# Optimization experiments

Measured on AMD Instinct MI355X. Metric: run time of the kernel, lower is better.

## Reference

```python
import jax, jax.numpy as jnp
import numpy as np

B, NA, NE = 1024, 15, 16
N_AGENTS = NA + 1
BN = B * N_AGENTS
D_OWN = D_ALL = D_EN = 32
H, NH, NMOVE, RD = 256, 4, 6, 8
HD = H // NH
GATE = 1.0
NEG = -1e9  # stand-in for -inf (safe under autodiff)


def _gelu(x):
    return jax.nn.gelu(x, approximate=False)  # torch nn.GELU default is exact


def _ln(x, g, b, eps=1e-5):
    m = x.mean(-1, keepdims=True)
    v = ((x - m) ** 2).mean(-1, keepdims=True)
    return (x - m) * jax.lax.rsqrt(v + eps) * g + b


def _masked_mean(x, mask, axis):
    w = mask[..., None].astype(x.dtype)
    return (x * w).sum(axis) / jnp.clip(w.sum(axis), 1e-8)


def _mha(q, kv, mask, Wq, Wk, Wv, Wo):
    # q: [BN,H], kv: [BN,M,H], mask: [BN,M] bool
    bn = q.shape[0]
    qh = (q @ Wq.T).reshape(bn, NH, HD)
    kh = (kv @ Wk.T).reshape(bn, -1, NH, HD)
    vh = (kv @ Wv.T).reshape(bn, -1, NH, HD)
    scores = jnp.einsum('bhd,bmhd->bhm', qh, kh) / np.sqrt(HD)
    scores = jnp.where(mask[:, None, :], scores, NEG)
    attn = jax.nn.softmax(scores, axis=-1)
    ctx = jnp.einsum('bhm,bmhd->bhd', attn, vh).reshape(bn, H)
    return ctx @ Wo.T


def setup_inputs() -> dict:
    key = jax.random.key(0)
    ks = iter(jax.random.split(key, 64))
    nrm = lambda *s: jax.random.normal(next(ks), s, dtype=jnp.float32)
    w = lambda o, i: nrm(o, i) * 0.02
    inp = dict(
        bs=B,
        own_feats=nrm(BN, 1, D_OWN),
        ally_feats=nrm(BN, NA, D_ALL),
        enemy_feats=nrm(BN, NE, D_EN),
        hidden_state=nrm(B, N_AGENTS, H),
        own_W=w(H, D_OWN), own_b=jnp.zeros(H),
        ally_W=w(H, D_ALL), ally_b=jnp.zeros(H),
        en_W=w(H, D_EN), en_b=jnp.zeros(H),
        aA_Wq=w(H, H), aA_Wk=w(H, H), aA_Wv=w(H, H), aA_Wo=w(H, H),
        aE_Wq=w(H, H), aE_Wk=w(H, H), aE_Wv=w(H, H), aE_Wo=w(H, H),
        fuse_W1=w(H, 3 * H), fuse_b1=jnp.zeros(H), fuse_g1=jnp.ones(H), fuse_be1=jnp.zeros(H),
        fuse_W2=w(H, H), fuse_b2=jnp.zeros(H),
        pool_W1=w(128, 3 * H), pool_b1=jnp.zeros(128), pool_g1=jnp.ones(128), pool_be1=jnp.zeros(128),
        pool_W2=w(128, 128), pool_b2=jnp.zeros(128),
        role_W1=w(128, 128), role_b1=jnp.zeros(128), role_g1=jnp.ones(128), role_be1=jnp.zeros(128),
        role_W2=w(RD, 128), role_b2=jnp.zeros(RD),
        rln_g=jnp.ones(RD), rln_b=jnp.zeros(RD),
        gru_Wih=w(3 * H, H + RD), gru_Whh=w(3 * H, H),
        gru_bih=jnp.zeros(3 * H), gru_bhh=jnp.zeros(3 * H),
        qn_W=w(NMOVE, H), qn_b=jnp.zeros(NMOVE),
        qp_W=w(H, H + RD), kp_W=w(H, H),
    )
    return inp


def reference(bs, own_feats, ally_feats, enemy_feats, hidden_state,
              own_W, own_b, ally_W, ally_b, en_W, en_b,
              aA_Wq, aA_Wk, aA_Wv, aA_Wo, aE_Wq, aE_Wk, aE_Wv, aE_Wo,
              fuse_W1, fuse_b1, fuse_g1, fuse_be1, fuse_W2, fuse_b2,
              pool_W1, pool_b1, pool_g1, pool_be1, pool_W2, pool_b2,
              role_W1, role_b1, role_g1, role_be1, role_W2, role_b2,
              rln_g, rln_b, gru_Wih, gru_Whh, gru_bih, gru_bhh,
              qn_W, qn_b, qp_W, kp_W):
    ally_mask = ~jnp.all(ally_feats == 0, axis=-1)   # [BN,Na]
    enemy_mask = ~jnp.all(enemy_feats == 0, axis=-1)  # [BN,Ne]

    own_e = own_feats @ own_W.T + own_b        # [BN,1,H]
    ally_e = ally_feats @ ally_W.T + ally_b    # [BN,Na,H]
    enemy_e = enemy_feats @ en_W.T + en_b      # [BN,Ne,H]
    self_emb = own_e[:, 0]                     # [BN,H]

    cA = _mha(self_emb, ally_e, ally_mask, aA_Wq, aA_Wk, aA_Wv, aA_Wo)
    cE = _mha(self_emb, enemy_e, enemy_mask, aE_Wq, aE_Wk, aE_Wv, aE_Wo)

    # fuse MLP: Linear -> GELU -> LN -> Linear
    f_in = jnp.concatenate([self_emb, cA, cE], axis=-1)
    h0 = _ln(_gelu(f_in @ fuse_W1.T + fuse_b1), fuse_g1, fuse_be1) @ fuse_W2.T + fuse_b2

    pA = _masked_mean(ally_e, ally_mask, 1)
    pE = _masked_mean(enemy_e, enemy_mask, 1)
    p_in = jnp.concatenate([self_emb, pA, pE], axis=-1)
    pooled = _ln(_gelu(p_in @ pool_W1.T + pool_b1), pool_g1, pool_be1) @ pool_W2.T + pool_b2
    r = jnp.tanh(_ln(_gelu(pooled @ role_W1.T + role_b1), role_g1, role_be1) @ role_W2.T + role_b2)
    r = _ln(r, rln_g, rln_b)

    # GRUCell (torch convention)
    h_prev = hidden_state.reshape(-1, H)
    x = jnp.concatenate([h0, GATE * r], axis=-1)
    gi = x @ gru_Wih.T + gru_bih
    gh = h_prev @ gru_Whh.T + gru_bhh
    i_r, i_z, i_n = jnp.split(gi, 3, axis=-1)
    h_r, h_z, h_n = jnp.split(gh, 3, axis=-1)
    rg = jax.nn.sigmoid(i_r + h_r)
    zg = jax.nn.sigmoid(i_z + h_z)
    ng = jnp.tanh(i_n + rg * h_n)
    h_cur = (1.0 - zg) * ng + zg * h_prev

    q_normal = h_cur @ qn_W.T + qn_b  # [BN,n_move]

    q_vec = jnp.concatenate([h_cur, GATE * r], axis=-1) @ qp_W.T  # [BN,H]
    k_vec = enemy_e @ kp_W.T                                       # [BN,Ne,H]
    logits = jnp.einsum('bj,bmj->bm', q_vec, k_vec) / np.sqrt(H)
    logits = jnp.where(enemy_mask, logits, NEG)
    denom = jnp.clip(enemy_mask.sum(-1, keepdims=True), 1).astype(logits.dtype)
    mean_valid = jnp.where(enemy_mask, logits, 0.0).sum(-1, keepdims=True) / denom
    q_interact = logits - mean_valid

    Q = jnp.concatenate([q_normal, q_interact], axis=-1)
    h_out = h_cur.reshape(bs, N_AGENTS, H)
    return Q, h_out
```

## Files before the change

kernel.cpp:

```cpp
#include <hip/hip_runtime.h>
#include <hip/hip_bf16.h>


#define MROWS 16384

typedef __attribute__((ext_vector_type(8))) short short8;
typedef __attribute__((ext_vector_type(4))) float float4v;
typedef __attribute__((ext_vector_type(4))) unsigned short ushort4v;
typedef __attribute__((ext_vector_type(2))) unsigned short ushort2v;

__device__ __forceinline__ unsigned short f2b(float f) {
    __hip_bfloat16 h = __float2bfloat16(f);
    return *reinterpret_cast<unsigned short*>(&h);
}
__device__ __forceinline__ float b2f(unsigned short u) {
    __hip_bfloat16 h;
    *reinterpret_cast<unsigned short*>(&h) = u;
    return __bfloat162float(h);
}
__device__ __forceinline__ void gll16(const unsigned short* g, unsigned short* l) {
    __builtin_amdgcn_global_load_lds((const __attribute__((address_space(1))) void*)g,
                                     (__attribute__((address_space(3))) void*)l, 16, 0, 0);
}

__global__ void cvt_misc(const float* __restrict__ hidden, const float* __restrict__ ownf,
                         unsigned short* __restrict__ XG, unsigned short* __restrict__ OWNb,
                         unsigned short* __restrict__ zbuf) {
    int idx = blockIdx.x * 256 + threadIdx.x;
    const int nh = MROWS * 64;
    const int no = MROWS * 8;
    if (idx < nh) {
        int row = idx >> 6, c4 = (idx & 63) * 4;
        float4 v = *(const float4*)(hidden + (size_t)row * 256 + c4);
        ushort4v d = { f2b(v.x), f2b(v.y), f2b(v.z), f2b(v.w) };
        *(ushort4v*)(XG + (size_t)row * 520 + 264 + c4) = d;
    } else if (idx < nh + no) {
        int j = idx - nh;
        int row = j >> 3, c4 = (j & 7) * 4;
        float4 v = *(const float4*)(ownf + (size_t)row * 32 + c4);
        ushort4v d = { f2b(v.x), f2b(v.y), f2b(v.z), f2b(v.w) };
        *(ushort4v*)(OWNb + (size_t)row * 32 + c4) = d;
    } else if (idx < nh + no + 16) {
        int j = idx - nh - no;
        ((uint4*)zbuf)[j] = make_uint4(0u, 0u, 0u, 0u);
    }
}

struct TOp {
    int type;
    const float* A; int sAi, sAk;
    const float* B; int sBj, sBk;
    void* O; int sOi;
    int I, J, K;
    int nb; int aB, bB, oB;
};
struct TOpSet { int n; int tiles[26]; TOp ops[26]; };

__global__ __launch_bounds__(256)
void compose_tiled(TOpSet S) {
    int t = blockIdx.x;
    int op = 0;
    while (op < S.n && t >= S.tiles[op]) { t -= S.tiles[op]; op++; }
    if (op >= S.n) return;
    TOp o = S.ops[op];
    int ti = (o.I + 31) >> 5, tj = (o.J + 31) >> 5;
    int per = ti * tj;
    int b = t / per;
    int rem = t - b * per;
    int i0 = (rem / tj) * 32, j0 = (rem % tj) * 32;
    int tid = threadIdx.x;
    if (o.type >= 2) {
        for (int e = tid; e < 1024; e += 256) {
            int r = e >> 5, c = e & 31;
            int i = i0 + r, j = j0 + c;
            if (i < o.I && j < o.J) {
                unsigned short v = 0;
                if (o.type == 2) v = f2b(o.A[(long)b * o.aB + (long)i * o.sAi + (long)j * o.sAk]);
                ((unsigned short*)o.O)[(long)b * o.oB + (long)i * o.sOi + j] = v;
            }
        }
        return;
    }
    __shared__ float As[32][33];
    __shared__ float Bs[32][33];
    int tx = tid & 15, ty = tid >> 4;
    float a00 = 0.f, a01 = 0.f, a10 = 0.f, a11 = 0.f;
    const float* Ab = o.A + (long)b * o.aB;
    const float* Bb = o.B + (long)b * o.bB;
    for (int k0 = 0; k0 < o.K; k0 += 32) {
        for (int e = tid; e < 1024; e += 256) {
            int r = e >> 5, c = e & 31;
            As[r][c] = (i0 + r < o.I && k0 + c < o.K)
                       ? Ab[(long)(i0 + r) * o.sAi + (long)(k0 + c) * o.sAk] : 0.f;
            Bs[r][c] = (k0 + r < o.K && j0 + c < o.J)
                       ? Bb[(long)(j0 + c) * o.sBj + (long)(k0 + r) * o.sBk] : 0.f;
        }
        __syncthreads();
#pragma unroll
        for (int k = 0; k < 32; k++) {
            float x0 = As[ty * 2][k], x1 = As[ty * 2 + 1][k];
            float y0 = Bs[k][tx * 2], y1 = Bs[k][tx * 2 + 1];
            a00 += x0 * y0; a01 += x0 * y1; a10 += x1 * y0; a11 += x1 * y1;
        }
        __syncthreads();
    }
    int i = i0 + ty * 2, j = j0 + tx * 2;
    float vals[2][2] = {{a00, a01}, {a10, a11}};
#pragma unroll
    for (int di = 0; di < 2; di++)
#pragma unroll
        for (int dj = 0; dj < 2; dj++) {
            int ii = i + di, jj = j + dj;
            if (ii < o.I && jj < o.J) {
                long oidx = (long)b * o.oB + (long)ii * o.sOi + jj;
                if (o.type == 0) ((unsigned short*)o.O)[oidx] = f2b(vals[di][dj]);
                else ((float*)o.O)[oidx] = vals[di][dj];
            }
        }
}

struct MOp { const float* A; int sAi; const float* x; const float* b1; const float* b2; float* out; int I, K; };
struct MOpSet { int n; int waves[10]; MOp ops[10]; };

__global__ void mv_ops(MOpSet S) {
    int wid = blockIdx.x * 4 + (threadIdx.x >> 6);
    int lane = threadIdx.x & 63;
    int op = 0;
    while (op < S.n && wid >= S.waves[op]) { wid -= S.waves[op]; op++; }
    if (op >= S.n) return;
    MOp o = S.ops[op];
    float s = 0.f;
    for (int k = lane; k < o.K; k += 64) s += o.A[(long)wid * o.sAi + k] * o.x[k];
    for (int off = 32; off; off >>= 1) s += __shfl_xor(s, off, 64);
    if (lane == 0) {
        if (o.b1) s += o.b1[wid];
        if (o.b2) s += o.b2[wid];
        o.out[wid] = s;
    }
}

template<int BM, int BN>
__global__ __launch_bounds__(256, 4)
void gemm_bf16(const unsigned short* __restrict__ A, int lda,
               const unsigned short* __restrict__ W,
               const float* __restrict__ bias,
               unsigned short* __restrict__ C, int ldc,
               int N, int K, int act,
               const unsigned short* __restrict__ zbuf) {
    constexpr int MI = BM / 32, NJ = BN / 32;
    __shared__ __align__(16) unsigned short As[2][BM * 32];
    __shared__ __align__(16) unsigned short Bs[2][BN * 32];
    int tid = threadIdx.x;
    int m0 = blockIdx.x * BM, n0 = blockIdx.y * BN;
    int wave = tid >> 6, lane = tid & 63;
    int wm = (wave & 1) * (BM / 2), wn = (wave >> 1) * (BN / 2);
    int l16 = lane & 15, quad = lane >> 4;

    float4v acc[MI][NJ];
#pragma unroll
    for (int i = 0; i < MI; i++)
#pragma unroll
        for (int j = 0; j < NJ; j++) acc[i][j] = (float4v){0.f, 0.f, 0.f, 0.f};

    int swz = ((l16 >> 1) & 3) * 8;
    int nt = (K + 31) >> 5;

    auto stage = [&](int buf, int k0) {
#pragma unroll
        for (int s0 = 0; s0 < BM * 4; s0 += 256) {
            int s = s0 + tid;
            int row = s >> 2;
            int cg = (s & 3) ^ ((row >> 1) & 3);
            int ka = k0 + cg * 8;
            gll16((ka < K) ? A + (size_t)(m0 + row) * lda + ka : zbuf, &As[buf][s * 8]);
        }
#pragma unroll
        for (int s0 = 0; s0 < BN * 4; s0 += 256) {
            int s = s0 + tid;
            int row = s >> 2;
            int cg = (s & 3) ^ ((row >> 1) & 3);
            int ka = k0 + cg * 8;
            gll16((ka < K && n0 + row < N) ? W + (size_t)(n0 + row) * K + ka : zbuf,
                  &Bs[buf][s * 8]);
        }
    };
    auto compute = [&](int buf) {
        short8 a[MI], b[NJ];
#pragma unroll
        for (int i = 0; i < MI; i++)
            a[i] = *(const short8*)(&As[buf][(wm + i * 16 + l16) * 32 + ((quad * 8) ^ swz)]);
#pragma unroll
        for (int j = 0; j < NJ; j++)
            b[j] = *(const short8*)(&Bs[buf][(wn + j * 16 + l16) * 32 + ((quad * 8) ^ swz)]);
#pragma unroll
        for (int i = 0; i < MI; i++)
#pragma unroll
            for (int j = 0; j < NJ; j++)
                acc[i][j] = __builtin_amdgcn_mfma_f32_16x16x32_bf16(a[i], b[j], acc[i][j], 0, 0, 0);
    };

    stage(0, 0);
    asm volatile("s_waitcnt vmcnt(0)" ::: "memory");
    __builtin_amdgcn_s_barrier();
    for (int t = 0; t < nt - 1; t++) {
        stage((t + 1) & 1, (t + 1) << 5);
        compute(t & 1);
        asm volatile("s_waitcnt vmcnt(0)" ::: "memory");
        __builtin_amdgcn_s_barrier();
    }
    compute((nt - 1) & 1);

#pragma unroll
    for (int i = 0; i < MI; i++) {
#pragma unroll
        for (int j = 0; j < NJ; j++) {
#pragma unroll
            for (int rr = 0; rr < 4; rr++) {
                int rowm = m0 + wm + i * 16 + quad * 4 + rr;
                int coln = wn + j * 16 + l16;
                if (n0 + coln >= N) continue;
                float v = acc[i][j][rr];
                if (bias) v += bias[n0 + coln];
                if (act == 1) v = 0.5f * v * (1.f + erff(v * 0.70710678f));
                C[(size_t)rowm * ldc + n0 + coln] = f2b(v);
            }
        }
    }
}

__global__ __launch_bounds__(256, 4)
void gemm_gru(const unsigned short* __restrict__ A, int lda,
              const unsigned short* __restrict__ W,
              const float* __restrict__ gbias,
              const float* __restrict__ hp,
              float* __restrict__ hout, unsigned short* __restrict__ XQ,
              int K, const unsigned short* __restrict__ zbuf) {
    __shared__ __align__(16) unsigned short As[2][64 * 32];
    __shared__ __align__(16) unsigned short Ws[2][4 * 64 * 32];
    int tid = threadIdx.x;
    int m0 = blockIdx.x * 64, n0 = blockIdx.y * 64;
    int wave = tid >> 6, lane = tid & 63;
    int wm = (wave & 1) * 32, wn = (wave >> 1) * 32;
    int l16 = lane & 15, quad = lane >> 4;

    float4v acc[4][2][2];
#pragma unroll
    for (int g = 0; g < 4; g++)
#pragma unroll
        for (int i = 0; i < 2; i++)
#pragma unroll
            for (int j = 0; j < 2; j++) acc[g][i][j] = (float4v){0.f, 0.f, 0.f, 0.f};

    int swz = ((l16 >> 1) & 3) * 8;
    int nt = (K + 31) >> 5;
    int srow = tid >> 2;
    int cg = (tid & 3) ^ ((srow >> 1) & 3);
    const unsigned short* Arow = A + (size_t)(m0 + srow) * lda + cg * 8;
    const unsigned short* Wrow[4];
#pragma unroll
    for (int g = 0; g < 4; g++)
        Wrow[g] = W + (size_t)(g * 256 + n0 + srow) * K + cg * 8;
    int kaOff = cg * 8;

    auto stage = [&](int buf, int k0) {
        int ka = k0 + kaOff;
        gll16((ka < K) ? Arow + k0 : zbuf, &As[buf][tid * 8]);
#pragma unroll
        for (int g = 0; g < 4; g++)
            gll16((ka < K) ? Wrow[g] + k0 : zbuf, &Ws[buf][(g * 256 + tid) * 8]);
    };
    auto compute = [&](int buf) {
        short8 a[2], b[4][2];
#pragma unroll
        for (int i = 0; i < 2; i++)
            a[i] = *(const short8*)(&As[buf][(wm + i * 16 + l16) * 32 + ((quad * 8) ^ swz)]);
#pragma unroll
        for (int g = 0; g < 4; g++)
#pragma unroll
            for (int j = 0; j < 2; j++)
                b[g][j] = *(const short8*)(&Ws[buf][g * 2048 + (wn + j * 16 + l16) * 32 + ((quad * 8) ^ swz)]);
#pragma unroll
        for (int g = 0; g < 4; g++)
#pragma unroll
            for (int i = 0; i < 2; i++)
#pragma unroll
                for (int j = 0; j < 2; j++)
                    acc[g][i][j] = __builtin_amdgcn_mfma_f32_16x16x32_bf16(a[i], b[g][j], acc[g][i][j], 0, 0, 0);
    };

    stage(0, 0);
    asm volatile("s_waitcnt vmcnt(0)" ::: "memory");
    __builtin_amdgcn_s_barrier();
    for (int t = 0; t < nt - 1; t++) {
        stage((t + 1) & 1, (t + 1) << 5);
        compute(t & 1);
        asm volatile("s_waitcnt vmcnt(0)" ::: "memory");
        __builtin_amdgcn_s_barrier();
    }
    compute((nt - 1) & 1);

#pragma unroll
    for (int i = 0; i < 2; i++) {
#pragma unroll
        for (int j = 0; j < 2; j++) {
#pragma unroll
            for (int rr = 0; rr < 4; rr++) {
                int rowm = m0 + wm + i * 16 + quad * 4 + rr;
                int coln = n0 + wn + j * 16 + l16;
                float r_ = acc[0][i][j][rr] + gbias[coln];
                float z_ = acc[1][i][j][rr] + gbias[256 + coln];
                float in_ = acc[2][i][j][rr] + gbias[512 + coln];
                float hn_ = acc[3][i][j][rr] + gbias[768 + coln];
                float rg = 1.f / (1.f + __expf(-r_));
                float zg = 1.f / (1.f + __expf(-z_));
                float ng = tanhf(in_ + rg * hn_);
                float h = (1.f - zg) * ng + zg * hp[(size_t)rowm * 256 + coln];
                hout[(size_t)rowm * 256 + coln] = h;
                XQ[(size_t)rowm * 264 + coln] = f2b(h);
            }
        }
    }
}

__global__ __launch_bounds__(256)
void ln_fp(const unsigned short* __restrict__ FPC,
           const float* __restrict__ g1, const float* __restrict__ be1,
           const float* __restrict__ g2, const float* __restrict__ be2,
           unsigned short* __restrict__ XG, unsigned short* __restrict__ T2) {
    int tid = threadIdx.x;
    size_t row = (size_t)blockIdx.x * 4 + (tid >> 6);
    int l = tid & 63;
    const unsigned short* src = FPC + row * 384;
    ushort4v vf = *(const ushort4v*)(src + l * 4);
    ushort2v vp = *(const ushort2v*)(src + 256 + l * 2);
    float f0 = b2f(vf[0]), f1 = b2f(vf[1]), f2v = b2f(vf[2]), f3 = b2f(vf[3]);
    float p0 = b2f(vp[0]), p1 = b2f(vp[1]);
    float s = f0 + f1 + f2v + f3;
    float q = f0 * f0 + f1 * f1 + f2v * f2v + f3 * f3;
    float s2 = p0 + p1, q2 = p0 * p0 + p1 * p1;
    for (int o = 32; o; o >>= 1) {
        s += __shfl_xor(s, o, 64); q += __shfl_xor(q, o, 64);
        s2 += __shfl_xor(s2, o, 64); q2 += __shfl_xor(q2, o, 64);
    }
    float mean = s * (1.f / 256.f);
    float rstd = rsqrtf(q * (1.f / 256.f) - mean * mean + 1e-5f);
    float4 g = *(const float4*)(g1 + l * 4);
    float4 be = *(const float4*)(be1 + l * 4);
    ushort4v o4;
    o4[0] = f2b((f0 - mean) * rstd * g.x + be.x);
    o4[1] = f2b((f1 - mean) * rstd * g.y + be.y);
    o4[2] = f2b((f2v - mean) * rstd * g.z + be.z);
    o4[3] = f2b((f3 - mean) * rstd * g.w + be.w);
    *(ushort4v*)(XG + row * 520 + l * 4) = o4;
    float mean2 = s2 * (1.f / 128.f);
    float rstd2 = rsqrtf(q2 * (1.f / 128.f) - mean2 * mean2 + 1e-5f);
    float2 gg = *(const float2*)(g2 + l * 2);
    float2 bb = *(const float2*)(be2 + l * 2);
    ushort2v o2;
    o2[0] = f2b((p0 - mean2) * rstd2 * gg.x + bb.x);
    o2[1] = f2b((p1 - mean2) * rstd2 * gg.y + bb.y);
    *(ushort2v*)(T2 + row * 128 + l * 2) = o2;
}

__global__ __launch_bounds__(256)
void glue_attn(const float* __restrict__ allyf, const float* __restrict__ enemyf,
               const float* __restrict__ ownf, const unsigned short* __restrict__ QKS,
               unsigned short* __restrict__ X) {
    __shared__ __align__(16) float af[4][540];
    __shared__ __align__(16) float ef[4][576];
    __shared__ __align__(16) float qk[4][288];
    __shared__ float attnA[4][64];
    __shared__ float attnE[4][64];
    __shared__ float mskA[4][16];
    __shared__ float mskE[4][16];
    int tid = threadIdx.x;
    size_t rb = (size_t)blockIdx.x * 4;

    for (int idx = tid; idx < 480; idx += 256) {
        int r = idx / 120, ch = idx - r * 120;
        float4 v = *(const float4*)(allyf + ((rb + r) * 480 + ch * 4));
        *(float4*)&af[r][(ch >> 3) * 36 + (ch & 7) * 4] = v;
    }
    for (int idx = tid; idx < 512; idx += 256) {
        int r = idx >> 7, ch = idx & 127;
        float4 v = *(const float4*)(enemyf + ((rb + r) * 512 + ch * 4));
        *(float4*)&ef[r][(ch >> 3) * 36 + (ch & 7) * 4] = v;
    }
    if (tid < 128) {
        int r = tid >> 5, ch = tid & 31;
        short8 v = *(const short8*)(QKS + (rb + r) * 256 + ch * 8);
#pragma unroll
        for (int j = 0; j < 8; j++)
            qk[r][(ch >> 2) * 36 + (ch & 3) * 8 + j] = b2f((unsigned short)v[j]);
    } else {
        int r = (tid - 128) >> 5, c = (tid - 128) & 31;
        X[(rb + r) * 360 + c] = f2b(ownf[(rb + r) * 32 + c]);
    }
    if (tid < 24) {
        int r = tid / 6, c = 98 + tid % 6;
        X[(rb + r) * 360 + c] = 0;
    }
    __syncthreads();

    if (tid < 248) {
        int pair = tid >> 1, half = tid & 1;
        int r = pair / 31, e = pair - r * 31;
        const float* base = (e < 15) ? &af[r][e * 36] : &ef[r][(e - 15) * 36];
        const float4* b4 = (const float4*)base + half * 4;
        bool nz = false;
#pragma unroll
        for (int k = 0; k < 4; k++) {
            float4 v = b4[k];
            nz |= (v.x != 0.f) || (v.y != 0.f) || (v.z != 0.f) || (v.w != 0.f);
        }
        int other = __shfl_xor((int)nz, 1, 64);
        float mv = (nz || other != 0) ? 1.f : 0.f;
        if (half == 0) {
            if (e < 15) mskA[r][e] = mv; else mskE[r][e - 15] = mv;
        }
    } else if (tid < 252) {
        mskA[tid - 248][15] = 0.f;
    }
    __syncthreads();

    int r = tid >> 6, lane = tid & 63;
    int h = lane >> 4, m = lane & 15;
    {
        float sc = -3.0e38f;
        if (m < 15) {
            const float4* qa = (const float4*)&qk[r][h * 36];
            const float4* aa = (const float4*)&af[r][m * 36];
            float s = 0.f;
#pragma unroll
            for (int k = 0; k < 8; k++) {
                float4 q = qa[k], a = aa[k];
                s += q.x * a.x + q.y * a.y + q.z * a.z + q.w * a.w;
            }
            sc = (mskA[r][m] > 0.f) ? s * 0.125f : -1e9f;
        }
        float mx = sc;
        for (int o = 8; o; o >>= 1) mx = fmaxf(mx, __shfl_xor(mx, o, 64));
        float e = (m < 15) ? __expf(sc - mx) : 0.f;
        float sm = e;
        for (int o = 8; o; o >>= 1) sm += __shfl_xor(sm, o, 64);
        attnA[r][h * 16 + m] = e / sm;
    }
    {
        const float4* qa = (const float4*)&qk[r][(4 + h) * 36];
        const float4* aa = (const float4*)&ef[r][m * 36];
        float s = 0.f;
#pragma unroll
        for (int k = 0; k < 8; k++) {
            float4 q = qa[k], a = aa[k];
            s += q.x * a.x + q.y * a.y + q.z * a.z + q.w * a.w;
        }
        float sc = (mskE[r][m] > 0.f) ? s * 0.125f : -1e9f;
        float mx = sc;
        for (int o = 8; o; o >>= 1) mx = fmaxf(mx, __shfl_xor(mx, o, 64));
        float e = __expf(sc - mx);
        float sm = e;
        for (int o = 8; o; o >>= 1) sm += __shfl_xor(sm, o, 64);
        attnE[r][h * 16 + m] = e / sm;
    }
    __syncthreads();
    size_t row = rb + r;
#pragma unroll
    for (int it = 0; it < 2; it++) {
        int idx = lane + it * 64;
        int hh = idx >> 5, c = idx & 31;
        float sA = 0.f;
        for (int mm = 0; mm < 15; mm++) sA += attnA[r][hh * 16 + mm] * af[r][mm * 36 + c];
        X[row * 360 + 104 + idx] = f2b(sA);
        float sE = 0.f;
        for (int mm = 0; mm < 16; mm++) sE += attnE[r][hh * 16 + mm] * ef[r][mm * 36 + c];
        X[row * 360 + 232 + idx] = f2b(sE);
    }
    if (lane < 32) {
        float cnt = 0.f;
        for (int mm = 0; mm < 15; mm++) cnt += mskA[r][mm];
        float s = 0.f;
        for (int mm = 0; mm < 15; mm++) s += af[r][mm * 36 + lane];
        X[row * 360 + 32 + lane] = f2b(s / fmaxf(cnt, 1e-8f));
        if (lane == 0) X[row * 360 + 96] = f2b(cnt > 0.f ? 1.f : 0.f);
    } else {
        int c = lane - 32;
        float cnt = 0.f;
        for (int mm = 0; mm < 16; mm++) cnt += mskE[r][mm];
        float s = 0.f;
        for (int mm = 0; mm < 16; mm++) s += ef[r][mm * 36 + c];
        X[row * 360 + 64 + c] = f2b(s / fmaxf(cnt, 1e-8f));
        if (c == 0) X[row * 360 + 97] = f2b(cnt > 0.f ? 1.f : 0.f);
    }
}

__global__ __launch_bounds__(256)
void ln_role(const unsigned short* __restrict__ T3, const float* __restrict__ g1,
             const float* __restrict__ be1, const float* __restrict__ W2,
             const float* __restrict__ b2, const float* __restrict__ rg,
             const float* __restrict__ rb, unsigned short* __restrict__ XG,
             unsigned short* __restrict__ XQ) {
    __shared__ float t3[32][132];
    __shared__ float gl[128], bl[128];
    int tid = threadIdx.x;
    size_t base = (size_t)blockIdx.x * 4096;
    for (int idx = tid; idx < 4096; idx += 256)
        t3[idx >> 7][idx & 127] = b2f(T3[base + idx]);
    if (tid < 128) { gl[tid] = g1[tid]; bl[tid] = be1[tid]; }
    __syncthreads();
    int r = tid >> 3, t = tid & 7;
    float s = 0.f, q = 0.f;
    for (int c = 0; c < 16; c++) { float v = t3[r][t * 16 + c]; s += v; q += v * v; }
    for (int o = 4; o; o >>= 1) { s += __shfl_xor(s, o, 8); q += __shfl_xor(q, o, 8); }
    float mean = s * (1.f / 128.f);
    float var = q * (1.f / 128.f) - mean * mean;
    float rstd = rsqrtf(var + 1e-5f);
    float acc = b2[t];
    const float* w = W2 + t * 128;
    for (int d = 0; d < 128; d++)
        acc += w[d] * ((t3[r][d] - mean) * rstd * gl[d] + bl[d]);
    float v = tanhf(acc);
    float mn = v;
    for (int o = 4; o; o >>= 1) mn += __shfl_xor(mn, o, 8);
    mn *= 0.125f;
    float dv = v - mn, qq = dv * dv;
    for (int o = 4; o; o >>= 1) qq += __shfl_xor(qq, o, 8);
    qq *= 0.125f;
    size_t row = (size_t)blockIdx.x * 32 + r;
    unsigned short ov = f2b(dv * rsqrtf(qq + 1e-5f) * rg[t] + rb[t]);
    XG[row * 520 + 256 + t] = ov;
    XQ[row * 264 + 256 + t] = ov;
}

__global__ __launch_bounds__(256)
void glue_final(const unsigned short* __restrict__ QWS, const float* __restrict__ efeats,
                const float* __restrict__ qnb, float* __restrict__ Q) {
    __shared__ __align__(16) float ef[8][576];
    __shared__ __align__(16) float qw[8][40];
    int tid = threadIdx.x;
    size_t rb = (size_t)blockIdx.x * 8;
    for (int idx = tid; idx < 1024; idx += 256) {
        int r = idx >> 7, ch = idx & 127;
        float4 v = *(const float4*)(efeats + (rb + r) * 512 + ch * 4);
        *(float4*)&ef[r][(ch >> 3) * 36 + (ch & 7) * 4] = v;
    }
    for (int idx = tid; idx < 320; idx += 256) {
        int r = idx / 40, c = idx % 40;
        qw[r][c] = b2f(QWS[(rb + r) * 40 + c]);
    }
    __syncthreads();
    int r = tid >> 5, t = tid & 31;
    size_t row = rb + r;
    float lg = 0.f, mk = 0.f;
    if (t < 16) {
        const float4* fr = (const float4*)&ef[r][t * 36];
        const float4* qv = (const float4*)&qw[r][0];
        bool nz = false;
        float s = 0.f;
#pragma unroll
        for (int k = 0; k < 8; k++) {
            float4 a = fr[k], b = qv[k];
            nz |= (a.x != 0.f) || (a.y != 0.f) || (a.z != 0.f) || (a.w != 0.f);
            s += a.x * b.x + a.y * b.y + a.z * b.z + a.w * b.w;
        }
        mk = nz ? 1.f : 0.f;
        lg = (s + qw[r][32]) * 0.0625f;
    }
    float sv = mk * lg, cv = mk;
    for (int o = 8; o; o >>= 1) { sv += __shfl_xor(sv, o, 64); cv += __shfl_xor(cv, o, 64); }
    float mean = sv / fmaxf(cv, 1.f);
    if (t < 16) Q[row * 22 + 6 + t] = (mk > 0.f ? lg : -1e9f) - mean;
    if (t < 6) Q[row * 22 + t] = qw[r][33 + t] + qnb[t];
}

extern "C" void kernel_launch(void* const* d_in, const int* in_sizes, int n_in,
                              void* d_out, int out_size, void* d_ws, size_t ws_size,
                              hipStream_t stream) {
    const float* own_feats = (const float*)d_in[1];
    const float* ally_feats = (const float*)d_in[2];
    const float* enemy_feats = (const float*)d_in[3];
    const float* hidden = (const float*)d_in[4];
    const float* own_W = (const float*)d_in[5];   const float* own_b = (const float*)d_in[6];
    const float* ally_W = (const float*)d_in[7];  const float* ally_b = (const float*)d_in[8];
    const float* en_W = (const float*)d_in[9];    const float* en_b = (const float*)d_in[10];
    const float* aA_Wq = (const float*)d_in[11];  const float* aA_Wk = (const float*)d_in[12];
    const float* aA_Wv = (const float*)d_in[13];  const float* aA_Wo = (const float*)d_in[14];
    const float* aE_Wq = (const float*)d_in[15];  const float* aE_Wk = (const float*)d_in[16];
    const float* aE_Wv = (const float*)d_in[17];  const float* aE_Wo = (const float*)d_in[18];
    const float* fuse_W1 = (const float*)d_in[19]; const float* fuse_b1 = (const float*)d_in[20];
    const float* fuse_g1 = (const float*)d_in[21]; const float* fuse_be1 = (const float*)d_in[22];
    const float* fuse_W2 = (const float*)d_in[23]; const float* fuse_b2 = (const float*)d_in[24];
    const float* pool_W1 = (const float*)d_in[25]; const float* pool_b1 = (const float*)d_in[26];
    const float* pool_g1 = (const float*)d_in[27]; const float* pool_be1 = (const float*)d_in[28];
    const float* pool_W2 = (const float*)d_in[29]; const float* pool_b2 = (const float*)d_in[30];
    const float* role_W1 = (const float*)d_in[31]; const float* role_b1 = (const float*)d_in[32];
    const float* role_g1 = (const float*)d_in[33]; const float* role_be1 = (const float*)d_in[34];
    const float* role_W2 = (const float*)d_in[35]; const float* role_b2 = (const float*)d_in[36];
    const float* rln_g = (const float*)d_in[37];   const float* rln_b = (const float*)d_in[38];
    const float* gru_Wih = (const float*)d_in[39]; const float* gru_Whh = (const float*)d_in[40];
    const float* gru_bih = (const float*)d_in[41]; const float* gru_bhh = (const float*)d_in[42];
    const float* qn_W = (const float*)d_in[43];    const float* qn_b = (const float*)d_in[44];
    const float* qp_W = (const float*)d_in[45];    const float* kp_W = (const float*)d_in[46];

    char* wsp = (char*)d_ws;
    size_t off = 0;
    auto alloc = [&](size_t bytes) { void* p = wsp + off; off = (off + bytes + 255) & ~(size_t)255; return p; };

    unsigned short* X    = (unsigned short*)alloc((size_t)MROWS * 360 * 2);
    unsigned short* XG   = (unsigned short*)alloc((size_t)MROWS * 520 * 2);
    unsigned short* FPC  = (unsigned short*)alloc((size_t)MROWS * 384 * 2);
    unsigned short* XQ   = (unsigned short*)alloc((size_t)MROWS * 264 * 2);
    unsigned short* T2b  = (unsigned short*)alloc((size_t)MROWS * 128 * 2);
    unsigned short* T3b  = (unsigned short*)alloc((size_t)MROWS * 128 * 2);
    unsigned short* QKSb = (unsigned short*)alloc((size_t)MROWS * 256 * 2);
    unsigned short* QWSb = (unsigned short*)alloc((size_t)MROWS * 40 * 2);
    unsigned short* OWNb = (unsigned short*)alloc((size_t)MROWS * 32 * 2);
    unsigned short* FPW  = (unsigned short*)alloc(384 * 360 * 2);
    unsigned short* WGRU = (unsigned short*)alloc(1024 * 520 * 2);
    unsigned short* QWSW = (unsigned short*)alloc(40 * 264 * 2);
    unsigned short* WQKSO= (unsigned short*)alloc(256 * 32 * 2);
    unsigned short* rpW  = (unsigned short*)alloc(128 * 128 * 2);
    unsigned short* zbuf = (unsigned short*)alloc(256);
    float* WkAp = (float*)alloc(256 * 32 * 4);
    float* WvAp = (float*)alloc(256 * 32 * 4);
    float* WkEp = (float*)alloc(256 * 32 * 4);
    float* WvEp = (float*)alloc(256 * 32 * 4);
    float* Wkpp = (float*)alloc(256 * 32 * 4);
    float* WQKS_AE = (float*)alloc(256 * 256 * 4);
    float* WoVA = (float*)alloc(256 * 128 * 4);
    float* WoVE = (float*)alloc(256 * 128 * 4);
    float* bvAp = (float*)alloc(256 * 4);
    float* bvEp = (float*)alloc(256 * 4);
    float* bkpp = (float*)alloc(256 * 4);
    float* vall = (float*)alloc(768 * 4);
    float* qksb = (float*)alloc(256 * 4);
    float* fpb  = (float*)alloc(384 * 4);
    float* gbias= (float*)alloc(1024 * 4);
    float* rpb  = (float*)alloc(128 * 4);

    float* Qout = (float*)d_out;
    float* Hout = Qout + (size_t)MROWS * 22;

    auto tilesOf = [](const TOp& o) {
        return o.nb * (((o.I + 31) / 32) * ((o.J + 31) / 32));
    };

    cvt_misc<<<(MROWS * 64 + MROWS * 8 + 16 + 255) / 256, 256, 0, stream>>>(hidden, own_feats, XG, OWNb, zbuf);

    {
        MOpSet S; S.n = 5; int waves = 0;
        S.ops[0] = {aA_Wv, 256, ally_b, nullptr, nullptr, bvAp, 256, 256};
        S.ops[1] = {aE_Wv, 256, en_b, nullptr, nullptr, bvEp, 256, 256};
        S.ops[2] = {kp_W, 256, en_b, nullptr, nullptr, bkpp, 256, 256};
        S.ops[3] = {nullptr, 0, nullptr, own_b, nullptr, vall, 256, 0};
        S.ops[4] = {role_W1, 128, pool_b2, role_b1, nullptr, rpb, 128, 128};
        for (int i = 0; i < S.n; i++) { S.waves[i] = S.ops[i].I; waves += S.ops[i].I; }
        mv_ops<<<(waves + 3) / 4, 256, 0, stream>>>(S);
    }
    {
        TOpSet S; S.n = 0; int grid = 0;
        auto add = [&](TOp o) { S.tiles[S.n] = tilesOf(o); grid += S.tiles[S.n]; S.ops[S.n++] = o; };
        add({1, aA_Wk, 256, 1, ally_W, 1, 32, WkAp, 32, 256, 32, 256, 1, 0, 0, 0});
        add({1, aA_Wv, 256, 1, ally_W, 1, 32, WvAp, 32, 256, 32, 256, 1, 0, 0, 0});
        add({1, aE_Wk, 256, 1, en_W, 1, 32, WkEp, 32, 256, 32, 256, 1, 0, 0, 0});
        add({1, aE_Wv, 256, 1, en_W, 1, 32, WvEp, 32, 256, 32, 256, 1, 0, 0, 0});
        add({1, kp_W, 256, 1, en_W, 1, 32, Wkpp, 32, 256, 32, 256, 1, 0, 0, 0});
        compose_tiled<<<grid, 256, 0, stream>>>(S);
    }
    {
        TOpSet S; S.n = 0; int grid = 0;
        auto add = [&](TOp o) { S.tiles[S.n] = tilesOf(o); grid += S.tiles[S.n]; S.ops[S.n++] = o; };
        add({1, WkAp, 1, 32, aA_Wq, 1, 256, WQKS_AE, 256, 32, 256, 64, 4, 2048, 16384, 8192});
        add({1, WkEp, 1, 32, aE_Wq, 1, 256, WQKS_AE + 128 * 256, 256, 32, 256, 64, 4, 2048, 16384, 8192});
        add({1, aA_Wo, 256, 1, WvAp, 1, 32, WoVA, 128, 256, 32, 64, 4, 64, 2048, 32});
        add({1, aE_Wo, 256, 1, WvEp, 1, 32, WoVE, 128, 256, 32, 64, 4, 64, 2048, 32});
        compose_tiled<<<grid, 256, 0, stream>>>(S);
    }
    {
        MOpSet S; S.n = 3; int waves = 0;
        S.ops[0] = {aA_Wo, 256, bvAp, nullptr, nullptr, vall + 256, 256, 256};
        S.ops[1] = {aE_Wo, 256, bvEp, nullptr, nullptr, vall + 512, 256, 256};
        S.ops[2] = {WQKS_AE, 256, own_b, nullptr, nullptr, qksb, 256, 256};
        for (int i = 0; i < S.n; i++) { S.waves[i] = S.ops[i].I; waves += S.ops[i].I; }
        mv_ops<<<(waves + 3) / 4, 256, 0, stream>>>(S);
    }
    {
        MOpSet S; S.n = 5; int waves = 0;
        S.ops[0] = {fuse_W1, 768, vall, fuse_b1, nullptr, fpb, 256, 768};
        S.ops[1] = {pool_W1, 768, vall, pool_b1, nullptr, fpb + 256, 128, 256};
        S.ops[2] = {gru_Wih, 264, fuse_b2, gru_bih, gru_bhh, gbias, 512, 256};
        S.ops[3] = {gru_Wih + 512 * 264, 264, fuse_b2, gru_bih + 512, nullptr, gbias + 512, 256, 256};
        S.ops[4] = {nullptr, 0, nullptr, gru_bhh + 512, nullptr, gbias + 768, 256, 0};
        for (int i = 0; i < S.n; i++) { S.waves[i] = S.ops[i].I; waves += S.ops[i].I; }
        mv_ops<<<(waves + 3) / 4, 256, 0, stream>>>(S);
    }
    {
        TOpSet S; S.n = 0; int grid = 0;
        auto add = [&](TOp o) { S.tiles[S.n] = tilesOf(o); grid += S.tiles[S.n]; S.ops[S.n++] = o; };
        add({0, fuse_W1, 768, 1, own_W, 1, 32, FPW, 360, 256, 32, 256, 1, 0, 0, 0});
        add({3, nullptr, 0, 0, nullptr, 0, 0, FPW + 32, 360, 256, 72, 0, 1, 0, 0, 0});
        add({0, fuse_W1 + 256, 768, 1, WoVA, 1, 128, FPW + 104, 360, 256, 128, 256, 1, 0, 0, 0});
        add({0, fuse_W1 + 512, 768, 1, WoVE, 1, 128, FPW + 232, 360, 256, 128, 256, 1, 0, 0, 0});
        add({0, pool_W1, 768, 1, own_W, 1, 32, FPW + 256 * 360, 360, 128, 32, 256, 1, 0, 0, 0});
        add({0, pool_W1 + 256, 768, 1, ally_W, 1, 32, FPW + 256 * 360 + 32, 360, 128, 32, 256, 1, 0, 0, 0});
        add({0, pool_W1 + 512, 768, 1, en_W, 1, 32, FPW + 256 * 360 + 64, 360, 128, 32, 256, 1, 0, 0, 0});
        add({0, pool_W1 + 256, 768, 1, ally_b, 0, 1, FPW + 256 * 360 + 96, 360, 128, 1, 256, 1, 0, 0, 0});
        add({0, pool_W1 + 512, 768, 1, en_b, 0, 1, FPW + 256 * 360 + 97, 360, 128, 1, 256, 1, 0, 0, 0});
        add({3, nullptr, 0, 0, nullptr, 0, 0, FPW + 256 * 360 + 98, 360, 128, 262, 0, 1, 0, 0, 0});
        add({0, gru_Wih, 264, 1, fuse_W2, 1, 256, WGRU, 520, 512, 256, 256, 1, 0, 0, 0});
        add({2, gru_Wih + 256, 264, 1, nullptr, 0, 0, WGRU + 256, 520, 512, 8, 0, 1, 0, 0, 0});
        add({2, gru_Whh, 256, 1, nullptr, 0, 0, WGRU + 264, 520, 512, 256, 0, 1, 0, 0, 0});
        add({0, gru_Wih + 512 * 264, 264, 1, fuse_W2, 1, 256, WGRU + 512 * 520, 520, 256, 256, 256, 1, 0, 0, 0});
        add({2, gru_Wih + 512 * 264 + 256, 264, 1, nullptr, 0, 0, WGRU + 512 * 520 + 256, 520, 256, 8, 0, 1, 0, 0, 0});
        add({3, nullptr, 0, 0, nullptr, 0, 0, WGRU + 512 * 520 + 264, 520, 256, 256, 0, 1, 0, 0, 0});
        add({3, nullptr, 0, 0, nullptr, 0, 0, WGRU + 768 * 520, 520, 256, 264, 0, 1, 0, 0, 0});
        add({2, gru_Whh + 512 * 256, 256, 1, nullptr, 0, 0, WGRU + 768 * 520 + 264, 520, 256, 256, 0, 1, 0, 0, 0});
        add({0, Wkpp, 1, 32, qp_W, 1, 264, QWSW, 264, 32, 264, 256, 1, 0, 0, 0});
        add({0, bkpp, 0, 1, qp_W, 1, 264, QWSW + 32 * 264, 264, 1, 264, 256, 1, 0, 0, 0});
        add({2, qn_W, 256, 1, nullptr, 0, 0, QWSW + 33 * 264, 264, 6, 256, 0, 1, 0, 0, 0});
        add({3, nullptr, 0, 0, nullptr, 0, 0, QWSW + 33 * 264 + 256, 264, 6, 8, 0, 1, 0, 0, 0});
        add({3, nullptr, 0, 0, nullptr, 0, 0, QWSW + 39 * 264, 264, 1, 264, 0, 1, 0, 0, 0});
        add({0, WQKS_AE, 256, 1, own_W, 1, 32, WQKSO, 32, 256, 32, 256, 1, 0, 0, 0});
        add({0, role_W1, 128, 1, pool_W2, 1, 128, rpW, 128, 128, 128, 128, 1, 0, 0, 0});
        compose_tiled<<<grid, 256, 0, stream>>>(S);
    }

    auto gemm = [&](const unsigned short* A, int lda, const unsigned short* Wm, const float* bias,
                    unsigned short* C, int ldc, int N, int K, int act) {
        gemm_bf16<64, 64><<<dim3(MROWS / 64, (N + 63) / 64), 256, 0, stream>>>(
            A, lda, Wm, bias, C, ldc, N, K, act, zbuf);
    };

    gemm(OWNb, 32, WQKSO, qksb, QKSb, 256, 256, 32, 0);
    glue_attn<<<MROWS / 4, 256, 0, stream>>>(ally_feats, enemy_feats, own_feats, QKSb, X);
    gemm(X, 360, FPW, fpb, FPC, 384, 384, 360, 1);
    ln_fp<<<MROWS / 4, 256, 0, stream>>>(FPC, fuse_g1, fuse_be1, pool_g1, pool_be1, XG, T2b);
    gemm(T2b, 128, rpW, rpb, T3b, 128, 128, 128, 1);
    ln_role<<<MROWS / 32, 256, 0, stream>>>(T3b, role_g1, role_be1, role_W2, role_b2, rln_g, rln_b, XG, XQ);
    gemm_gru<<<dim3(MROWS / 64, 4), 256, 0, stream>>>(XG, 520, WGRU, gbias, hidden,
                                                      Hout, XQ, 520, zbuf);
    gemm(XQ, 264, QWSW, nullptr, QWSb, 40, 40, 264, 0);
    glue_final<<<MROWS / 8, 256, 0, stream>>>(QWSb, enemy_feats, qn_b, Qout);
}
```

Measured before the change: 413.8 us.

## Fuse own-feature QK projection into glue_attn and split GRU GEMM across eight waves

The small K=32 GEMM that projected own features into the query-key space is removed. Each glue_attn block now computes those 256 outputs per row directly from the bf16-rounded own features and the composed weight. This drops a kernel launch, the OWNb conversion pass and the QKS intermediate buffer round trip. Separately, gemm_gru now runs 512 threads per block with 8 waves, each owning 16 rows instead of 32, to raise parallelism and cut per-thread accumulator registers, at the cost of more waves sharing the same LDS tiles.

```diff
diff --git a/kernel.cpp b/kernel.cpp
--- a/kernel.cpp
+++ b/kernel.cpp
@@ -23,25 +23,18 @@
                                      (__attribute__((address_space(3))) void*)l, 16, 0, 0);
 }
 
-__global__ void cvt_misc(const float* __restrict__ hidden, const float* __restrict__ ownf,
-                         unsigned short* __restrict__ XG, unsigned short* __restrict__ OWNb,
+__global__ void cvt_misc(const float* __restrict__ hidden,
+                         unsigned short* __restrict__ XG,
                          unsigned short* __restrict__ zbuf) {
     int idx = blockIdx.x * 256 + threadIdx.x;
     const int nh = MROWS * 64;
-    const int no = MROWS * 8;
     if (idx < nh) {
         int row = idx >> 6, c4 = (idx & 63) * 4;
         float4 v = *(const float4*)(hidden + (size_t)row * 256 + c4);
         ushort4v d = { f2b(v.x), f2b(v.y), f2b(v.z), f2b(v.w) };
         *(ushort4v*)(XG + (size_t)row * 520 + 264 + c4) = d;
-    } else if (idx < nh + no) {
+    } else if (idx < nh + 16) {
         int j = idx - nh;
-        int row = j >> 3, c4 = (j & 7) * 4;
-        float4 v = *(const float4*)(ownf + (size_t)row * 32 + c4);
-        ushort4v d = { f2b(v.x), f2b(v.y), f2b(v.z), f2b(v.w) };
-        *(ushort4v*)(OWNb + (size_t)row * 32 + c4) = d;
-    } else if (idx < nh + no + 16) {
-        int j = idx - nh - no;
         ((uint4*)zbuf)[j] = make_uint4(0u, 0u, 0u, 0u);
     }
 }
@@ -228,7 +221,7 @@
     }
 }
 
-__global__ __launch_bounds__(256, 4)
+__global__ __launch_bounds__(512, 4)
 void gemm_gru(const unsigned short* __restrict__ A, int lda,
               const unsigned short* __restrict__ W,
               const float* __restrict__ gbias,
@@ -240,40 +233,53 @@
     int tid = threadIdx.x;
     int m0 = blockIdx.x * 64, n0 = blockIdx.y * 64;
     int wave = tid >> 6, lane = tid & 63;
-    int wm = (wave & 1) * 32, wn = (wave >> 1) * 32;
+    int wm = (wave & 3) * 16, wn = (wave >> 2) * 32;
     int l16 = lane & 15, quad = lane >> 4;
 
-    float4v acc[4][2][2];
+    float4v acc[4][2];
 #pragma unroll
     for (int g = 0; g < 4; g++)
 #pragma unroll
-        for (int i = 0; i < 2; i++)
-#pragma unroll
-            for (int j = 0; j < 2; j++) acc[g][i][j] = (float4v){0.f, 0.f, 0.f, 0.f};
+        for (int j = 0; j < 2; j++) acc[g][j] = (float4v){0.f, 0.f, 0.f, 0.f};
 
     int swz = ((l16 >> 1) & 3) * 8;
     int nt = (K + 31) >> 5;
-    int srow = tid >> 2;
-    int cg = (tid & 3) ^ ((srow >> 1) & 3);
-    const unsigned short* Arow = A + (size_t)(m0 + srow) * lda + cg * 8;
-    const unsigned short* Wrow[4];
-#pragma unroll
-    for (int g = 0; g < 4; g++)
-        Wrow[g] = W + (size_t)(g * 256 + n0 + srow) * K + cg * 8;
-    int kaOff = cg * 8;
+
+    const unsigned short* Aptr = A;
+    int aKoff = 0;
+    if (tid < 256) {
+        int row = tid >> 2;
+        int cg = (tid & 3) ^ ((row >> 1) & 3);
+        Aptr = A + (size_t)(m0 + row) * lda + cg * 8;
+        aKoff = cg * 8;
+    }
+    const unsigned short* Wptr[2];
+    int wKoff[2];
+    int wSlot0 = tid, wSlot1 = tid + 512;
+    {
+        int s = wSlot0;
+        int g = s >> 8, s8 = s & 255;
+        int row = s8 >> 2;
+        int cg = (s8 & 3) ^ ((row >> 1) & 3);
+        Wptr[0] = W + (size_t)(g * 256 + n0 + row) * K + cg * 8;
+        wKoff[0] = cg * 8;
+        s = wSlot1;
+        g = s >> 8; s8 = s & 255;
+        row = s8 >> 2;
+        cg = (s8 & 3) ^ ((row >> 1) & 3);
+        Wptr[1] = W + (size_t)(g * 256 + n0 + row) * K + cg * 8;
+        wKoff[1] = cg * 8;
+    }
 
     auto stage = [&](int buf, int k0) {
-        int ka = k0 + kaOff;
-        gll16((ka < K) ? Arow + k0 : zbuf, &As[buf][tid * 8]);
-#pragma unroll
-        for (int g = 0; g < 4; g++)
-            gll16((ka < K) ? Wrow[g] + k0 : zbuf, &Ws[buf][(g * 256 + tid) * 8]);
+        if (tid < 256)
+            gll16((k0 + aKoff < K) ? Aptr + k0 : zbuf, &As[buf][tid * 8]);
+        gll16((k0 + wKoff[0] < K) ? Wptr[0] + k0 : zbuf, &Ws[buf][wSlot0 * 8]);
+        gll16((k0 + wKoff[1] < K) ? Wptr[1] + k0 : zbuf, &Ws[buf][wSlot1 * 8]);
     };
     auto compute = [&](int buf) {
-        short8 a[2], b[4][2];
-#pragma unroll
-        for (int i = 0; i < 2; i++)
-            a[i] = *(const short8*)(&As[buf][(wm + i * 16 + l16) * 32 + ((quad * 8) ^ swz)]);
+        short8 a = *(const short8*)(&As[buf][(wm + l16) * 32 + ((quad * 8) ^ swz)]);
+        short8 b[4][2];
 #pragma unroll
         for (int g = 0; g < 4; g++)
 #pragma unroll
@@ -282,10 +288,8 @@
 #pragma unroll
         for (int g = 0; g < 4; g++)
 #pragma unroll
-            for (int i = 0; i < 2; i++)
-#pragma unroll
-                for (int j = 0; j < 2; j++)
-                    acc[g][i][j] = __builtin_amdgcn_mfma_f32_16x16x32_bf16(a[i], b[g][j], acc[g][i][j], 0, 0, 0);
+            for (int j = 0; j < 2; j++)
+                acc[g][j] = __builtin_amdgcn_mfma_f32_16x16x32_bf16(a, b[g][j], acc[g][j], 0, 0, 0);
     };
 
     stage(0, 0);
@@ -300,24 +304,21 @@
     compute((nt - 1) & 1);
 
 #pragma unroll
-    for (int i = 0; i < 2; i++) {
-#pragma unroll
-        for (int j = 0; j < 2; j++) {
-#pragma unroll
-            for (int rr = 0; rr < 4; rr++) {
-                int rowm = m0 + wm + i * 16 + quad * 4 + rr;
-                int coln = n0 + wn + j * 16 + l16;
-                float r_ = acc[0][i][j][rr] + gbias[coln];
-                float z_ = acc[1][i][j][rr] + gbias[256 + coln];
-                float in_ = acc[2][i][j][rr] + gbias[512 + coln];
-                float hn_ = acc[3][i][j][rr] + gbias[768 + coln];
-                float rg = 1.f / (1.f + __expf(-r_));
-                float zg = 1.f / (1.f + __expf(-z_));
-                float ng = tanhf(in_ + rg * hn_);
-                float h = (1.f - zg) * ng + zg * hp[(size_t)rowm * 256 + coln];
-                hout[(size_t)rowm * 256 + coln] = h;
-                XQ[(size_t)rowm * 264 + coln] = f2b(h);
-            }
+    for (int j = 0; j < 2; j++) {
+#pragma unroll
+        for (int rr = 0; rr < 4; rr++) {
+            int rowm = m0 + wm + quad * 4 + rr;
+            int coln = n0 + wn + j * 16 + l16;
+            float r_ = acc[0][j][rr] + gbias[coln];
+            float z_ = acc[1][j][rr] + gbias[256 + coln];
+            float in_ = acc[2][j][rr] + gbias[512 + coln];
+            float hn_ = acc[3][j][rr] + gbias[768 + coln];
+            float rg = 1.f / (1.f + __expf(-r_));
+            float zg = 1.f / (1.f + __expf(-z_));
+            float ng = tanhf(in_ + rg * hn_);
+            float h = (1.f - zg) * ng + zg * hp[(size_t)rowm * 256 + coln];
+            hout[(size_t)rowm * 256 + coln] = h;
+            XQ[(size_t)rowm * 264 + coln] = f2b(h);
         }
     }
 }
@@ -364,11 +365,12 @@
 
 __global__ __launch_bounds__(256)
 void glue_attn(const float* __restrict__ allyf, const float* __restrict__ enemyf,
-               const float* __restrict__ ownf, const unsigned short* __restrict__ QKS,
-               unsigned short* __restrict__ X) {
+               const float* __restrict__ ownf, const unsigned short* __restrict__ WQKSO,
+               const float* __restrict__ qksb, unsigned short* __restrict__ X) {
     __shared__ __align__(16) float af[4][540];
     __shared__ __align__(16) float ef[4][576];
     __shared__ __align__(16) float qk[4][288];
+    __shared__ float ow[4][32];
     __shared__ float attnA[4][64];
     __shared__ float attnE[4][64];
     __shared__ float mskA[4][16];
@@ -386,15 +388,11 @@
         float4 v = *(const float4*)(enemyf + ((rb + r) * 512 + ch * 4));
         *(float4*)&ef[r][(ch >> 3) * 36 + (ch & 7) * 4] = v;
     }
-    if (tid < 128) {
-        int r = tid >> 5, ch = tid & 31;
-        short8 v = *(const short8*)(QKS + (rb + r) * 256 + ch * 8);
-#pragma unroll
-        for (int j = 0; j < 8; j++)
-            qk[r][(ch >> 2) * 36 + (ch & 3) * 8 + j] = b2f((unsigned short)v[j]);
-    } else {
+    if (tid >= 128 && tid < 256) {
         int r = (tid - 128) >> 5, c = (tid - 128) & 31;
-        X[(rb + r) * 360 + c] = f2b(ownf[(rb + r) * 32 + c]);
+        unsigned short ob = f2b(ownf[(rb + r) * 32 + c]);
+        X[(rb + r) * 360 + c] = ob;
+        ow[r][c] = b2f(ob);
     }
     if (tid < 24) {
         int r = tid / 6, c = 98 + tid % 6;
@@ -420,6 +418,24 @@
         }
     } else if (tid < 252) {
         mskA[tid - 248][15] = 0.f;
+    }
+    {
+        int r = tid >> 6, cb = (tid & 63) * 4;
+        const float* owr = ow[r];
+#pragma unroll
+        for (int cc = 0; cc < 4; cc++) {
+            int c = cb + cc;
+            const unsigned short* wr = WQKSO + c * 32;
+            float s = qksb[c];
+#pragma unroll
+            for (int k = 0; k < 32; k += 8) {
+                short8 wv = *(const short8*)(wr + k);
+#pragma unroll
+                for (int j = 0; j < 8; j++)
+                    s += owr[k + j] * b2f((unsigned short)wv[j]);
+            }
+            qk[r][(c >> 5) * 36 + (c & 31)] = s;
+        }
     }
     __syncthreads();
 
@@ -611,9 +627,7 @@
     unsigned short* XQ   = (unsigned short*)alloc((size_t)MROWS * 264 * 2);
     unsigned short* T2b  = (unsigned short*)alloc((size_t)MROWS * 128 * 2);
     unsigned short* T3b  = (unsigned short*)alloc((size_t)MROWS * 128 * 2);
-    unsigned short* QKSb = (unsigned short*)alloc((size_t)MROWS * 256 * 2);
     unsigned short* QWSb = (unsigned short*)alloc((size_t)MROWS * 40 * 2);
-    unsigned short* OWNb = (unsigned short*)alloc((size_t)MROWS * 32 * 2);
     unsigned short* FPW  = (unsigned short*)alloc(384 * 360 * 2);
     unsigned short* WGRU = (unsigned short*)alloc(1024 * 520 * 2);
     unsigned short* QWSW = (unsigned short*)alloc(40 * 264 * 2);
@@ -644,7 +658,7 @@
         return o.nb * (((o.I + 31) / 32) * ((o.J + 31) / 32));
     };
 
-    cvt_misc<<<(MROWS * 64 + MROWS * 8 + 16 + 255) / 256, 256, 0, stream>>>(hidden, own_feats, XG, OWNb, zbuf);
+    cvt_misc<<<(MROWS * 64 + 16 + 255) / 256, 256, 0, stream>>>(hidden, XG, zbuf);
 
     {
         MOpSet S; S.n = 5; int waves = 0;
@@ -730,13 +744,12 @@
             A, lda, Wm, bias, C, ldc, N, K, act, zbuf);
     };
 
-    gemm(OWNb, 32, WQKSO, qksb, QKSb, 256, 256, 32, 0);
-    glue_attn<<<MROWS / 4, 256, 0, stream>>>(ally_feats, enemy_feats, own_feats, QKSb, X);
+    glue_attn<<<MROWS / 4, 256, 0, stream>>>(ally_feats, enemy_feats, own_feats, WQKSO, qksb, X);
     gemm(X, 360, FPW, fpb, FPC, 384, 384, 360, 1);
     ln_fp<<<MROWS / 4, 256, 0, stream>>>(FPC, fuse_g1, fuse_be1, pool_g1, pool_be1, XG, T2b);
     gemm(T2b, 128, rpW, rpb, T3b, 128, 128, 128, 1);
     ln_role<<<MROWS / 32, 256, 0, stream>>>(T3b, role_g1, role_be1, role_W2, role_b2, rln_g, rln_b, XG, XQ);
-    gemm_gru<<<dim3(MROWS / 64, 4), 256, 0, stream>>>(XG, 520, WGRU, gbias, hidden,
+    gemm_gru<<<dim3(MROWS / 64, 4), 512, 0, stream>>>(XG, 520, WGRU, gbias, hidden,
                                                       Hout, XQ, 520, zbuf);
     gemm(XQ, 264, QWSW, nullptr, QWSb, 40, 40, 264, 0);
     glue_final<<<MROWS / 8, 256, 0, stream>>>(QWSb, enemy_feats, qn_b, Qout);
```

New measurement: 421.2 us. About the same (+1.8%).
